# Optimization experiments

Measured on AMD Instinct MI355X. Metric: run time of the kernel, lower is better.

The kernel has to match this reference:

```python
import jax, jax.numpy as jnp
import numpy as np

N, E, D = 40000, 640000, 128
EPS = 1e-5


def _lin(k, out_d, in_d):
    s = 1.0 / np.sqrt(in_d)
    kw, kb = jax.random.split(k)
    W = jax.random.uniform(kw, (out_d, in_d), minval=-s, maxval=s, dtype=jnp.float32)
    b = jax.random.uniform(kb, (out_d,), minval=-s, maxval=s, dtype=jnp.float32)
    return W, b


def setup_inputs() -> dict:
    key = jax.random.key(0)
    kx, ke, k1, k2, k3, k4 = jax.random.split(key, 6)
    x = jax.random.normal(kx, (N, D), dtype=jnp.float32)
    edge_index = jax.random.randint(ke, (2, E), 0, N, dtype=jnp.int64)
    Wm1, bm1 = _lin(k1, D, D)
    Wm2, bm2 = _lin(k2, D, D)
    Wu1, bu1 = _lin(k3, D, 2 * D)
    Wu2, bu2 = _lin(k4, D, D)
    gamma = jnp.ones((D,), jnp.float32)
    beta = jnp.zeros((D,), jnp.float32)
    return dict(x=x, edge_index=edge_index, Wm1=Wm1, bm1=bm1, Wm2=Wm2, bm2=bm2,
                Wu1=Wu1, bu1=bu1, Wu2=Wu2, bu2=bu2, gamma=gamma, beta=beta)


def reference(x, edge_index, Wm1, bm1, Wm2, bm2, Wu1, bu1, Wu2, bu2, gamma, beta):
    num_nodes = x.shape[0]
    src, dst = edge_index[0], edge_index[1]
    # message MLP on gathered source features: (E, D)
    m = jax.nn.relu(x[src] @ Wm1.T + bm1) @ Wm2.T + bm2
    # scatter-mean via segment_sum + clamped count
    agg = jax.ops.segment_sum(m, dst, num_segments=num_nodes)
    cnt = jax.ops.segment_sum(jnp.ones((dst.shape[0],), m.dtype), dst, num_segments=num_nodes)
    agg = agg / jnp.clip(cnt, 1.0, None)[:, None]
    # update MLP on concat([x, agg]) -> (N, D); dropout is identity in eval
    comb = jnp.concatenate([x, agg], axis=-1)
    u = jax.nn.relu(comb @ Wu1.T + bu1) @ Wu2.T + bu2
    # residual + LayerNorm
    h = u + x
    mu = h.mean(-1, keepdims=True)
    var = ((h - mu) ** 2).mean(-1, keepdims=True)
    return (h - mu) / jnp.sqrt(var + EPS) * gamma + beta
```

## Files before the change

kernel.cpp:

```cpp
#include <hip/hip_runtime.h>

#define N_NODES 40000
#define N_EDGES 640000
#define DIM 128
#define NBLK_SCAN 157
#define NBLK_GEMM 313

typedef __bf16 bf16;
typedef __bf16 v8bf __attribute__((ext_vector_type(8)));
typedef __bf16 v4bf __attribute__((ext_vector_type(4)));
typedef float f32x4 __attribute__((ext_vector_type(4)));

#define MFMA(a, b, c) __builtin_amdgcn_mfma_f32_16x16x32_bf16(a, b, c, 0, 0, 0)

#define OFF_WM1 0
#define OFF_BM1 16384
#define OFF_WM2 16512
#define OFF_BM2 32896
#define OFF_WU1 33024
#define OFF_BU1 65792
#define OFF_WU2 65920
#define OFF_BU2 82304
#define OFF_GAM 82432
#define OFF_BET 82560
#define NPARAM  82688

template<bool I64>
__device__ __forceinline__ int ldi(const void* p, size_t i) {
    if constexpr (I64) return (int)((const long long*)p)[i];
    else               return ((const int*)p)[i];
}

__global__ __launch_bounds__(256) void detect_kernel(const unsigned short* __restrict__ xh,
                                                     const unsigned int* __restrict__ eiw,
                                                     int* __restrict__ flags) {
    __shared__ int sf[2];
    int tid = threadIdx.x;
    if (tid == 0) { sf[0] = 0; sf[1] = 0; }
    __syncthreads();
    int isf32 = 0; unsigned int orhi = 0;
    #pragma unroll
    for (int j = 0; j < 4; ++j) {
        unsigned short h = xh[2 * (tid + 256 * j)];
        if (((h >> 7) & 0xFF) >= 0xC0) isf32 = 1;
        orhi |= eiw[2 * (tid + 256 * j) + 1];
    }
    if (isf32) atomicOr(&sf[0], 1);
    if (orhi)  atomicOr(&sf[1], 1);
    __syncthreads();
    if (tid == 0) { flags[0] = sf[0]; flags[1] = sf[1] ? 0 : 1; }
}

__global__ __launch_bounds__(256) void convert_params_kernel(
    const void* Wm1, const void* bm1, const void* Wm2, const void* bm2,
    const void* Wu1, const void* bu1, const void* Wu2, const void* bu2,
    const void* gam, const void* bet, const int* __restrict__ flags,
    bf16* __restrict__ wp)
{
    int i = blockIdx.x * 256 + threadIdx.x;
    if (i >= NPARAM) return;
    const void* src; int base;
    if      (i < OFF_BM1) { src = Wm1; base = OFF_WM1; }
    else if (i < OFF_WM2) { src = bm1; base = OFF_BM1; }
    else if (i < OFF_BM2) { src = Wm2; base = OFF_WM2; }
    else if (i < OFF_WU1) { src = bm2; base = OFF_BM2; }
    else if (i < OFF_BU1) { src = Wu1; base = OFF_WU1; }
    else if (i < OFF_WU2) { src = bu1; base = OFF_BU1; }
    else if (i < OFF_BU2) { src = Wu2; base = OFF_WU2; }
    else if (i < OFF_GAM) { src = bu2; base = OFF_BU2; }
    else if (i < OFF_BET) { src = gam; base = OFF_GAM; }
    else                  { src = bet; base = OFF_BET; }
    int j = i - base;
    float v = flags[0] ? ((const float*)src)[j] : (float)((const bf16*)src)[j];
    wp[i] = (bf16)v;
}

__global__ __launch_bounds__(256) void convert_x_kernel(const void* __restrict__ x,
                                                        const int* __restrict__ flags,
                                                        bf16* __restrict__ xb) {
    const int NT = N_NODES * DIM;
    int stride = gridDim.x * 256;
    if (flags[0]) {
        const float4* g = (const float4*)x;
        v4bf* o = (v4bf*)xb;
        for (int i = blockIdx.x * 256 + threadIdx.x; i < NT / 4; i += stride) {
            float4 v = g[i];
            v4bf t; t[0] = (bf16)v.x; t[1] = (bf16)v.y; t[2] = (bf16)v.z; t[3] = (bf16)v.w;
            o[i] = t;
        }
    } else {
        const uint4* g = (const uint4*)x;
        uint4* o = (uint4*)xb;
        for (int i = blockIdx.x * 256 + threadIdx.x; i < NT / 8; i += stride) o[i] = g[i];
    }
}


__global__ __launch_bounds__(256) void msg_kernel(const bf16* __restrict__ xb,
                                                  const bf16* __restrict__ wp,
                                                  bf16* __restrict__ y)
{
    __shared__ __align__(16) bf16 sc[4][32 * DIM];
    const int wave = threadIdx.x >> 6, lane = threadIdx.x & 63;
    const int l15 = lane & 15, quad = lane >> 4;
    const int row0 = (blockIdx.x * 4 + wave) * 32;
    bf16* s = sc[wave];
    const bf16* W1 = wp + OFF_WM1;
    const bf16* W2 = wp + OFF_WM2;

    const int ra = min(row0 + l15, N_NODES - 1);
    const int rb = min(row0 + 16 + l15, N_NODES - 1);

    f32x4 acc[2][8] = {};
    #pragma unroll
    for (int kt = 0; kt < 4; ++kt) {
        int k0 = kt * 32 + quad * 8;
        v8bf a0 = *(const v8bf*)&xb[(size_t)ra * DIM + k0];
        v8bf a1 = *(const v8bf*)&xb[(size_t)rb * DIM + k0];
        #pragma unroll
        for (int ct = 0; ct < 8; ++ct) {
            v8bf b = *(const v8bf*)&W1[(ct * 16 + l15) * DIM + k0];
            acc[0][ct] = MFMA(a0, b, acc[0][ct]);
            acc[1][ct] = MFMA(a1, b, acc[1][ct]);
        }
    }
    #pragma unroll
    for (int ct = 0; ct < 8; ++ct) {
        float bb = (float)wp[OFF_BM1 + ct * 16 + l15];
        int c8w = (ct << 1) | (l15 >> 3);
        #pragma unroll
        for (int i = 0; i < 2; ++i)
            #pragma unroll
            for (int r = 0; r < 4; ++r) {
                int row = i * 16 + quad * 4 + r;
                s[row * DIM + (((c8w ^ (row & 15)) << 3) | (l15 & 7))] =
                    (bf16)fmaxf(acc[i][ct][r] + bb, 0.f);
            }
    }
    f32x4 acc2[2][8] = {};
    #pragma unroll
    for (int kt = 0; kt < 4; ++kt) {
        int k0 = kt * 32 + quad * 8;
        int c8 = kt * 4 + quad;
        v8bf a0 = *(const v8bf*)&s[l15 * DIM + ((c8 ^ l15) << 3)];
        v8bf a1 = *(const v8bf*)&s[(16 + l15) * DIM + ((c8 ^ l15) << 3)];
        #pragma unroll
        for (int ct = 0; ct < 8; ++ct) {
            v8bf b = *(const v8bf*)&W2[(ct * 16 + l15) * DIM + k0];
            acc2[0][ct] = MFMA(a0, b, acc2[0][ct]);
            acc2[1][ct] = MFMA(a1, b, acc2[1][ct]);
        }
    }
    #pragma unroll
    for (int ct = 0; ct < 8; ++ct) {
        float bb = (float)wp[OFF_BM2 + ct * 16 + l15];
        #pragma unroll
        for (int i = 0; i < 2; ++i)
            #pragma unroll
            for (int r = 0; r < 4; ++r) {
                int grow = row0 + i * 16 + quad * 4 + r;
                if (grow < N_NODES)
                    y[(size_t)grow * DIM + ct * 16 + l15] = (bf16)(acc2[i][ct][r] + bb);
            }
    }
}

__global__ __launch_bounds__(256) void update_kernel(const bf16* __restrict__ xb,
                                                     const bf16* __restrict__ agg,
                                                     const bf16* __restrict__ wp,
                                                     const int* __restrict__ flags,
                                                     void* __restrict__ out)
{
    __shared__ __align__(16) bf16 sc[4][32 * DIM];
    const int wave = threadIdx.x >> 6, lane = threadIdx.x & 63;
    const int l15 = lane & 15, quad = lane >> 4;
    const int row0 = (blockIdx.x * 4 + wave) * 32;
    bf16* s = sc[wave];
    const bf16* W1 = wp + OFF_WU1;
    const bf16* W2 = wp + OFF_WU2;
    const int of32 = flags[0];

    const int ra = min(row0 + l15, N_NODES - 1);
    const int rb = min(row0 + 16 + l15, N_NODES - 1);

    f32x4 acc[2][8] = {};
    #pragma unroll
    for (int kt = 0; kt < 8; ++kt) {
        int k0 = kt * 32 + quad * 8;
        const bf16* A = (kt < 4) ? xb : agg;
        int ko = (kt < 4) ? k0 : (k0 - 128);
        v8bf a0 = *(const v8bf*)&A[(size_t)ra * DIM + ko];
        v8bf a1 = *(const v8bf*)&A[(size_t)rb * DIM + ko];
        #pragma unroll
        for (int ct = 0; ct < 8; ++ct) {
            v8bf b = *(const v8bf*)&W1[(ct * 16 + l15) * 256 + k0];
            acc[0][ct] = MFMA(a0, b, acc[0][ct]);
            acc[1][ct] = MFMA(a1, b, acc[1][ct]);
        }
    }
    #pragma unroll
    for (int ct = 0; ct < 8; ++ct) {
        float bb = (float)wp[OFF_BU1 + ct * 16 + l15];
        int c8w = (ct << 1) | (l15 >> 3);
        #pragma unroll
        for (int i = 0; i < 2; ++i)
            #pragma unroll
            for (int r = 0; r < 4; ++r) {
                int row = i * 16 + quad * 4 + r;
                s[row * DIM + (((c8w ^ (row & 15)) << 3) | (l15 & 7))] =
                    (bf16)fmaxf(acc[i][ct][r] + bb, 0.f);
            }
    }
    f32x4 acc2[2][8] = {};
    #pragma unroll
    for (int kt = 0; kt < 4; ++kt) {
        int k0 = kt * 32 + quad * 8;
        int c8 = kt * 4 + quad;
        v8bf a0 = *(const v8bf*)&s[l15 * DIM + ((c8 ^ l15) << 3)];
        v8bf a1 = *(const v8bf*)&s[(16 + l15) * DIM + ((c8 ^ l15) << 3)];
        #pragma unroll
        for (int ct = 0; ct < 8; ++ct) {
            v8bf b = *(const v8bf*)&W2[(ct * 16 + l15) * DIM + k0];
            acc2[0][ct] = MFMA(a0, b, acc2[0][ct]);
            acc2[1][ct] = MFMA(a1, b, acc2[1][ct]);
        }
    }

    float bu2c[8], gc[8], bc[8];
    #pragma unroll
    for (int ct = 0; ct < 8; ++ct) {
        int col = ct * 16 + l15;
        bu2c[ct] = (float)wp[OFF_BU2 + col];
        gc[ct]   = (float)wp[OFF_GAM + col];
        bc[ct]   = (float)wp[OFF_BET + col];
    }
    #pragma unroll
    for (int i = 0; i < 2; ++i) {
        #pragma unroll
        for (int r = 0; r < 4; ++r) {
            int grow = row0 + i * 16 + quad * 4 + r;
            int growc = min(grow, N_NODES - 1);
            float u[8], s1 = 0.f, s2 = 0.f;
            #pragma unroll
            for (int ct = 0; ct < 8; ++ct) {
                float v = acc2[i][ct][r] + bu2c[ct]
                        + (float)xb[(size_t)growc * DIM + ct * 16 + l15];
                u[ct] = v; s1 += v; s2 += v * v;
            }
            #pragma unroll
            for (int off = 1; off < 16; off <<= 1) {
                s1 += __shfl_xor(s1, off);
                s2 += __shfl_xor(s2, off);
            }
            float mean = s1 * (1.f / 128.f);
            float var  = s2 * (1.f / 128.f) - mean * mean;
            float rstd = rsqrtf(var + 1e-5f);
            if (grow < N_NODES) {
                if (of32) {
                    #pragma unroll
                    for (int ct = 0; ct < 8; ++ct)
                        ((float*)out)[(size_t)grow * DIM + ct * 16 + l15] =
                            (u[ct] - mean) * rstd * gc[ct] + bc[ct];
                } else {
                    #pragma unroll
                    for (int ct = 0; ct < 8; ++ct)
                        ((bf16*)out)[(size_t)grow * DIM + ct * 16 + l15] =
                            (bf16)((u[ct] - mean) * rstd * gc[ct] + bc[ct]);
                }
            }
        }
    }
}

template<bool I64>
__device__ void hist_body(const void* ei, int* deg) {
    int e = blockIdx.x * 256 + threadIdx.x;
    if (e < N_EDGES) atomicAdd(&deg[ldi<I64>(ei, (size_t)N_EDGES + e)], 1);
}
__global__ __launch_bounds__(256) void hist_kernel(const void* ei, int* deg, const int* flags) {
    if (flags[1]) hist_body<true>(ei, deg); else hist_body<false>(ei, deg);
}

__global__ __launch_bounds__(256) void scan1_kernel(const int* __restrict__ deg,
                                                    int* __restrict__ bscan,
                                                    int* __restrict__ bsum) {
    __shared__ int s[256];
    int tid = threadIdx.x;
    int i = blockIdx.x * 256 + tid;
    int v = (i < N_NODES) ? deg[i] : 0;
    s[tid] = v;
    for (int off = 1; off < 256; off <<= 1) {
        __syncthreads();
        int t = (tid >= off) ? s[tid - off] : 0;
        __syncthreads();
        s[tid] += t;
    }
    if (i < N_NODES) bscan[i] = s[tid] - v;
    if (tid == 255) bsum[blockIdx.x] = s[255];
}

__global__ __launch_bounds__(256) void scan2_kernel(int* __restrict__ bsum) {
    __shared__ int s[256];
    int tid = threadIdx.x;
    int v = (tid < NBLK_SCAN) ? bsum[tid] : 0;
    s[tid] = v;
    for (int off = 1; off < 256; off <<= 1) {
        __syncthreads();
        int t = (tid >= off) ? s[tid - off] : 0;
        __syncthreads();
        s[tid] += t;
    }
    if (tid < NBLK_SCAN) bsum[tid] = s[tid] - v;
}

__global__ __launch_bounds__(256) void scan3_kernel(const int* __restrict__ bscan,
                                                    const int* __restrict__ bsum,
                                                    int* __restrict__ offsets) {
    int i = blockIdx.x * 256 + threadIdx.x;
    if (i < N_NODES) offsets[i] = bscan[i] + bsum[blockIdx.x];
}

template<bool I64>
__device__ void scatter_body(const void* ei, int* offsets, int* srcs) {
    int e = blockIdx.x * 256 + threadIdx.x;
    if (e < N_EDGES) {
        int d = ldi<I64>(ei, (size_t)N_EDGES + e);
        int pos = atomicAdd(&offsets[d], 1);
        srcs[pos] = ldi<I64>(ei, e);
    }
}
__global__ __launch_bounds__(256) void scatter_kernel(const void* ei, int* offsets, int* srcs,
                                                      const int* flags) {
    if (flags[1]) scatter_body<true>(ei, offsets, srcs);
    else          scatter_body<false>(ei, offsets, srcs);
}

__device__ __forceinline__ void accum8(float* s, uint4 v) {
    v8bf b = __builtin_bit_cast(v8bf, v);
    #pragma unroll
    for (int j = 0; j < 8; ++j) s[j] += (float)b[j];
}

__global__ __launch_bounds__(256) void agg_kernel(const bf16* __restrict__ y,
                                                  const int* __restrict__ srcs,
                                                  const int* __restrict__ offsets,
                                                  const int* __restrict__ deg,
                                                  bf16* __restrict__ agg) {
    const int node = (blockIdx.x << 2) + (threadIdx.x >> 6);
    const int lane = threadIdx.x & 63;
    const int slot = lane >> 4, c16 = lane & 15;
    const int end = offsets[node];
    const int cnt = deg[node];
    const int beg = end - cnt;
    const uint4* yv = (const uint4*)y;

    float s0[8] = {}, s1[8] = {};
    int e = beg + slot;
    for (; e + 4 < end; e += 8) {
        int i0 = srcs[e], i1 = srcs[e + 4];
        uint4 v0 = yv[(size_t)i0 * 16 + c16];
        uint4 v1 = yv[(size_t)i1 * 16 + c16];
        accum8(s0, v0);
        accum8(s1, v1);
    }
    if (e < end) accum8(s0, yv[(size_t)srcs[e] * 16 + c16]);

    float inv = 1.f / (float)(cnt > 0 ? cnt : 1);
    v8bf o;
    #pragma unroll
    for (int j = 0; j < 8; ++j) {
        float v = s0[j] + s1[j];
        v += __shfl_xor(v, 16);
        v += __shfl_xor(v, 32);
        o[j] = (bf16)(v * inv);
    }
    if (slot == 0)
        ((uint4*)agg)[(size_t)node * 16 + c16] = __builtin_bit_cast(uint4, o);
}

extern "C" void kernel_launch(void* const* d_in, const int* in_sizes, int n_in,
                              void* d_out, int out_size, void* d_ws, size_t ws_size,
                              hipStream_t stream) {
    const void* x   = d_in[0];
    const void* ei  = d_in[1];

    char* ws = (char*)d_ws;
    size_t off = 0;
    auto alloc = [&](size_t bytes) {
        void* p = ws + off;
        off += (bytes + 255) & ~(size_t)255;
        return p;
    };
    bf16* y       = (bf16*)alloc((size_t)N_NODES * DIM * sizeof(bf16));
    bf16* agg     = (bf16*)alloc((size_t)N_NODES * DIM * sizeof(bf16));
    bf16* xb      = (bf16*)alloc((size_t)N_NODES * DIM * sizeof(bf16));
    bf16* wp      = (bf16*)alloc((size_t)NPARAM * sizeof(bf16));
    int*  deg     = (int*)alloc(N_NODES * sizeof(int));
    int*  offsets = (int*)alloc(N_NODES * sizeof(int));
    int*  bscan   = (int*)alloc(N_NODES * sizeof(int));
    int*  bsum    = (int*)alloc(1024);
    int*  srcs    = (int*)alloc((size_t)N_EDGES * sizeof(int));
    int*  flags   = (int*)alloc(256);

    hipMemsetAsync(deg, 0, N_NODES * sizeof(int), stream);

    detect_kernel<<<1, 256, 0, stream>>>((const unsigned short*)x, (const unsigned int*)ei, flags);
    convert_params_kernel<<<(NPARAM + 255) / 256, 256, 0, stream>>>(
        d_in[2], d_in[3], d_in[4], d_in[5], d_in[6], d_in[7], d_in[8], d_in[9],
        d_in[10], d_in[11], flags, wp);
    convert_x_kernel<<<1024, 256, 0, stream>>>(x, flags, xb);

    msg_kernel<<<NBLK_GEMM, 256, 0, stream>>>(xb, wp, y);

    hist_kernel<<<(N_EDGES + 255) / 256, 256, 0, stream>>>(ei, deg, flags);
    scan1_kernel<<<NBLK_SCAN, 256, 0, stream>>>(deg, bscan, bsum);
    scan2_kernel<<<1, 256, 0, stream>>>(bsum);
    scan3_kernel<<<NBLK_SCAN, 256, 0, stream>>>(bscan, bsum, offsets);
    scatter_kernel<<<(N_EDGES + 255) / 256, 256, 0, stream>>>(ei, offsets, srcs, flags);
    agg_kernel<<<N_NODES / 4, 256, 0, stream>>>(y, srcs, offsets, deg, agg);

    update_kernel<<<NBLK_GEMM, 256, 0, stream>>>(xb, agg, wp, flags, d_out);
}
```

Before: 250.1 us.

## Fuse front-end prep and CSR build into one cooperative grid-synced kernel

```diff
diff --git a/kernel.cpp b/kernel.cpp
--- a/kernel.cpp
+++ b/kernel.cpp
@@ -1,10 +1,14 @@
 #include <hip/hip_runtime.h>
+#include <hip/hip_cooperative_groups.h>
+
+namespace cg = cooperative_groups;
 
 #define N_NODES 40000
 #define N_EDGES 640000
 #define DIM 128
 #define NBLK_SCAN 157
 #define NBLK_GEMM 313
+#define COOP_BLOCKS 256
 
 typedef __bf16 bf16;
 typedef __bf16 v8bf __attribute__((ext_vector_type(8)));
@@ -25,76 +29,136 @@
 #define OFF_BET 82560
 #define NPARAM  82688
 
-template<bool I64>
-__device__ __forceinline__ int ldi(const void* p, size_t i) {
-    if constexpr (I64) return (int)((const long long*)p)[i];
-    else               return ((const int*)p)[i];
-}
-
-__global__ __launch_bounds__(256) void detect_kernel(const unsigned short* __restrict__ xh,
-                                                     const unsigned int* __restrict__ eiw,
-                                                     int* __restrict__ flags) {
+__global__ __launch_bounds__(256) void coop_front_kernel(
+    const void* __restrict__ x, const void* __restrict__ ei,
+    const void* p0, const void* p1, const void* p2, const void* p3,
+    const void* p4, const void* p5, const void* p6, const void* p7,
+    const void* p8, const void* p9,
+    bf16* __restrict__ wp, bf16* __restrict__ xb,
+    int* __restrict__ deg, int* __restrict__ bscan, int* __restrict__ bsum,
+    int* __restrict__ offsets, int* __restrict__ srcs, int* __restrict__ flags)
+{
+    cg::grid_group grid = cg::this_grid();
     __shared__ int sf[2];
-    int tid = threadIdx.x;
+    __shared__ int s[256];
+    const int tid = threadIdx.x;
+    const int gid = blockIdx.x * 256 + tid;
+    const int gstride = gridDim.x * 256;
+
     if (tid == 0) { sf[0] = 0; sf[1] = 0; }
     __syncthreads();
-    int isf32 = 0; unsigned int orhi = 0;
-    #pragma unroll
-    for (int j = 0; j < 4; ++j) {
-        unsigned short h = xh[2 * (tid + 256 * j)];
-        if (((h >> 7) & 0xFF) >= 0xC0) isf32 = 1;
-        orhi |= eiw[2 * (tid + 256 * j) + 1];
-    }
-    if (isf32) atomicOr(&sf[0], 1);
-    if (orhi)  atomicOr(&sf[1], 1);
+    {
+        const unsigned short* xh = (const unsigned short*)x;
+        const unsigned int* eiw = (const unsigned int*)ei;
+        int isf32 = 0; unsigned int orhi = 0;
+        #pragma unroll
+        for (int j = 0; j < 4; ++j) {
+            unsigned short h = xh[2 * (tid + 256 * j)];
+            if (((h >> 7) & 0xFF) >= 0xC0) isf32 = 1;
+            orhi |= eiw[2 * (tid + 256 * j) + 1];
+        }
+        if (isf32) atomicOr(&sf[0], 1);
+        if (orhi)  atomicOr(&sf[1], 1);
+    }
     __syncthreads();
-    if (tid == 0) { flags[0] = sf[0]; flags[1] = sf[1] ? 0 : 1; }
-}
-
-__global__ __launch_bounds__(256) void convert_params_kernel(
-    const void* Wm1, const void* bm1, const void* Wm2, const void* bm2,
-    const void* Wu1, const void* bu1, const void* Wu2, const void* bu2,
-    const void* gam, const void* bet, const int* __restrict__ flags,
-    bf16* __restrict__ wp)
-{
-    int i = blockIdx.x * 256 + threadIdx.x;
-    if (i >= NPARAM) return;
-    const void* src; int base;
-    if      (i < OFF_BM1) { src = Wm1; base = OFF_WM1; }
-    else if (i < OFF_WM2) { src = bm1; base = OFF_BM1; }
-    else if (i < OFF_BM2) { src = Wm2; base = OFF_WM2; }
-    else if (i < OFF_WU1) { src = bm2; base = OFF_BM2; }
-    else if (i < OFF_BU1) { src = Wu1; base = OFF_WU1; }
-    else if (i < OFF_WU2) { src = bu1; base = OFF_BU1; }
-    else if (i < OFF_BU2) { src = Wu2; base = OFF_WU2; }
-    else if (i < OFF_GAM) { src = bu2; base = OFF_BU2; }
-    else if (i < OFF_BET) { src = gam; base = OFF_GAM; }
-    else                  { src = bet; base = OFF_BET; }
-    int j = i - base;
-    float v = flags[0] ? ((const float*)src)[j] : (float)((const bf16*)src)[j];
-    wp[i] = (bf16)v;
-}
-
-__global__ __launch_bounds__(256) void convert_x_kernel(const void* __restrict__ x,
-                                                        const int* __restrict__ flags,
-                                                        bf16* __restrict__ xb) {
-    const int NT = N_NODES * DIM;
-    int stride = gridDim.x * 256;
-    if (flags[0]) {
-        const float4* g = (const float4*)x;
-        v4bf* o = (v4bf*)xb;
-        for (int i = blockIdx.x * 256 + threadIdx.x; i < NT / 4; i += stride) {
-            float4 v = g[i];
-            v4bf t; t[0] = (bf16)v.x; t[1] = (bf16)v.y; t[2] = (bf16)v.z; t[3] = (bf16)v.w;
-            o[i] = t;
-        }
+    const int f32m = sf[0];
+    const int i64m = sf[1] ? 0 : 1;
+    if (blockIdx.x == 0 && tid == 0) { flags[0] = f32m; flags[1] = i64m; }
+
+    for (int i = gid; i < NPARAM; i += gstride) {
+        const void* src; int base;
+        if      (i < OFF_BM1) { src = p0; base = OFF_WM1; }
+        else if (i < OFF_WM2) { src = p1; base = OFF_BM1; }
+        else if (i < OFF_BM2) { src = p2; base = OFF_WM2; }
+        else if (i < OFF_WU1) { src = p3; base = OFF_BM2; }
+        else if (i < OFF_BU1) { src = p4; base = OFF_WU1; }
+        else if (i < OFF_WU2) { src = p5; base = OFF_BU1; }
+        else if (i < OFF_BU2) { src = p6; base = OFF_WU2; }
+        else if (i < OFF_GAM) { src = p7; base = OFF_BU2; }
+        else if (i < OFF_BET) { src = p8; base = OFF_GAM; }
+        else                  { src = p9; base = OFF_BET; }
+        int j = i - base;
+        float v = f32m ? ((const float*)src)[j] : (float)((const bf16*)src)[j];
+        wp[i] = (bf16)v;
+    }
+    {
+        const int NT = N_NODES * DIM;
+        if (f32m) {
+            const float4* g = (const float4*)x;
+            v4bf* o = (v4bf*)xb;
+            for (int i = gid; i < NT / 4; i += gstride) {
+                float4 v = g[i];
+                v4bf t; t[0] = (bf16)v.x; t[1] = (bf16)v.y; t[2] = (bf16)v.z; t[3] = (bf16)v.w;
+                o[i] = t;
+            }
+        } else {
+            const uint4* g = (const uint4*)x;
+            uint4* o = (uint4*)xb;
+            for (int i = gid; i < NT / 8; i += gstride) o[i] = g[i];
+        }
+    }
+    for (int i = gid; i < N_NODES; i += gstride) deg[i] = 0;
+    grid.sync();
+
+    if (i64m) {
+        const long long* d = (const long long*)ei + N_EDGES;
+        for (int e = gid; e < N_EDGES; e += gstride) atomicAdd(&deg[(int)d[e]], 1);
     } else {
-        const uint4* g = (const uint4*)x;
-        uint4* o = (uint4*)xb;
-        for (int i = blockIdx.x * 256 + threadIdx.x; i < NT / 8; i += stride) o[i] = g[i];
-    }
-}
-
+        const int* d = (const int*)ei + N_EDGES;
+        for (int e = gid; e < N_EDGES; e += gstride) atomicAdd(&deg[d[e]], 1);
+    }
+    grid.sync();
+
+    if (blockIdx.x < NBLK_SCAN) {
+        int i = blockIdx.x * 256 + tid;
+        int v = (i < N_NODES) ? deg[i] : 0;
+        s[tid] = v;
+        for (int off = 1; off < 256; off <<= 1) {
+            __syncthreads();
+            int t = (tid >= off) ? s[tid - off] : 0;
+            __syncthreads();
+            s[tid] += t;
+        }
+        if (i < N_NODES) bscan[i] = s[tid] - v;
+        if (tid == 255) bsum[blockIdx.x] = s[255];
+    }
+    grid.sync();
+
+    if (blockIdx.x == 0) {
+        int v = (tid < NBLK_SCAN) ? bsum[tid] : 0;
+        s[tid] = v;
+        for (int off = 1; off < 256; off <<= 1) {
+            __syncthreads();
+            int t = (tid >= off) ? s[tid - off] : 0;
+            __syncthreads();
+            s[tid] += t;
+        }
+        if (tid < NBLK_SCAN) bsum[tid] = s[tid] - v;
+    }
+    grid.sync();
+
+    for (int i = gid; i < N_NODES; i += gstride)
+        offsets[i] = bscan[i] + bsum[i >> 8];
+    grid.sync();
+
+    if (i64m) {
+        const long long* sp = (const long long*)ei;
+        const long long* dp = sp + N_EDGES;
+        for (int e = gid; e < N_EDGES; e += gstride) {
+            int d = (int)dp[e];
+            int pos = atomicAdd(&offsets[d], 1);
+            srcs[pos] = (int)sp[e];
+        }
+    } else {
+        const int* sp = (const int*)ei;
+        const int* dp = sp + N_EDGES;
+        for (int e = gid; e < N_EDGES; e += gstride) {
+            int d = dp[e];
+            int pos = atomicAdd(&offsets[d], 1);
+            srcs[pos] = sp[e];
+        }
+    }
+}
 
 __global__ __launch_bounds__(256) void msg_kernel(const bf16* __restrict__ xb,
                                                   const bf16* __restrict__ wp,
@@ -272,69 +336,6 @@
     }
 }
 
-template<bool I64>
-__device__ void hist_body(const void* ei, int* deg) {
-    int e = blockIdx.x * 256 + threadIdx.x;
-    if (e < N_EDGES) atomicAdd(&deg[ldi<I64>(ei, (size_t)N_EDGES + e)], 1);
-}
-__global__ __launch_bounds__(256) void hist_kernel(const void* ei, int* deg, const int* flags) {
-    if (flags[1]) hist_body<true>(ei, deg); else hist_body<false>(ei, deg);
-}
-
-__global__ __launch_bounds__(256) void scan1_kernel(const int* __restrict__ deg,
-                                                    int* __restrict__ bscan,
-                                                    int* __restrict__ bsum) {
-    __shared__ int s[256];
-    int tid = threadIdx.x;
-    int i = blockIdx.x * 256 + tid;
-    int v = (i < N_NODES) ? deg[i] : 0;
-    s[tid] = v;
-    for (int off = 1; off < 256; off <<= 1) {
-        __syncthreads();
-        int t = (tid >= off) ? s[tid - off] : 0;
-        __syncthreads();
-        s[tid] += t;
-    }
-    if (i < N_NODES) bscan[i] = s[tid] - v;
-    if (tid == 255) bsum[blockIdx.x] = s[255];
-}
-
-__global__ __launch_bounds__(256) void scan2_kernel(int* __restrict__ bsum) {
-    __shared__ int s[256];
-    int tid = threadIdx.x;
-    int v = (tid < NBLK_SCAN) ? bsum[tid] : 0;
-    s[tid] = v;
-    for (int off = 1; off < 256; off <<= 1) {
-        __syncthreads();
-        int t = (tid >= off) ? s[tid - off] : 0;
-        __syncthreads();
-        s[tid] += t;
-    }
-    if (tid < NBLK_SCAN) bsum[tid] = s[tid] - v;
-}
-
-__global__ __launch_bounds__(256) void scan3_kernel(const int* __restrict__ bscan,
-                                                    const int* __restrict__ bsum,
-                                                    int* __restrict__ offsets) {
-    int i = blockIdx.x * 256 + threadIdx.x;
-    if (i < N_NODES) offsets[i] = bscan[i] + bsum[blockIdx.x];
-}
-
-template<bool I64>
-__device__ void scatter_body(const void* ei, int* offsets, int* srcs) {
-    int e = blockIdx.x * 256 + threadIdx.x;
-    if (e < N_EDGES) {
-        int d = ldi<I64>(ei, (size_t)N_EDGES + e);
-        int pos = atomicAdd(&offsets[d], 1);
-        srcs[pos] = ldi<I64>(ei, e);
-    }
-}
-__global__ __launch_bounds__(256) void scatter_kernel(const void* ei, int* offsets, int* srcs,
-                                                      const int* flags) {
-    if (flags[1]) scatter_body<true>(ei, offsets, srcs);
-    else          scatter_body<false>(ei, offsets, srcs);
-}
-
 __device__ __forceinline__ void accum8(float* s, uint4 v) {
     v8bf b = __builtin_bit_cast(v8bf, v);
     #pragma unroll
@@ -381,8 +382,8 @@
 extern "C" void kernel_launch(void* const* d_in, const int* in_sizes, int n_in,
                               void* d_out, int out_size, void* d_ws, size_t ws_size,
                               hipStream_t stream) {
-    const void* x   = d_in[0];
-    const void* ei  = d_in[1];
+    const void* x  = d_in[0];
+    const void* ei = d_in[1];
 
     char* ws = (char*)d_ws;
     size_t off = 0;
@@ -402,22 +403,23 @@
     int*  srcs    = (int*)alloc((size_t)N_EDGES * sizeof(int));
     int*  flags   = (int*)alloc(256);
 
-    hipMemsetAsync(deg, 0, N_NODES * sizeof(int), stream);
-
-    detect_kernel<<<1, 256, 0, stream>>>((const unsigned short*)x, (const unsigned int*)ei, flags);
-    convert_params_kernel<<<(NPARAM + 255) / 256, 256, 0, stream>>>(
-        d_in[2], d_in[3], d_in[4], d_in[5], d_in[6], d_in[7], d_in[8], d_in[9],
-        d_in[10], d_in[11], flags, wp);
-    convert_x_kernel<<<1024, 256, 0, stream>>>(x, flags, xb);
+    void* p0 = (void*)d_in[2]; void* p1 = (void*)d_in[3];
+    void* p2 = (void*)d_in[4]; void* p3 = (void*)d_in[5];
+    void* p4 = (void*)d_in[6]; void* p5 = (void*)d_in[7];
+    void* p6 = (void*)d_in[8]; void* p7 = (void*)d_in[9];
+    void* p8 = (void*)d_in[10]; void* p9 = (void*)d_in[11];
+
+    void* args[] = {
+        (void*)&x, (void*)&ei,
+        (void*)&p0, (void*)&p1, (void*)&p2, (void*)&p3, (void*)&p4,
+        (void*)&p5, (void*)&p6, (void*)&p7, (void*)&p8, (void*)&p9,
+        (void*)&wp, (void*)&xb, (void*)&deg, (void*)&bscan, (void*)&bsum,
+        (void*)&offsets, (void*)&srcs, (void*)&flags
+    };
+    hipLaunchCooperativeKernel((void*)coop_front_kernel, dim3(COOP_BLOCKS),
+                               dim3(256), args, 0, stream);
 
     msg_kernel<<<NBLK_GEMM, 256, 0, stream>>>(xb, wp, y);
-
-    hist_kernel<<<(N_EDGES + 255) / 256, 256, 0, stream>>>(ei, deg, flags);
-    scan1_kernel<<<NBLK_SCAN, 256, 0, stream>>>(deg, bscan, bsum);
-    scan2_kernel<<<1, 256, 0, stream>>>(bsum);
-    scan3_kernel<<<NBLK_SCAN, 256, 0, stream>>>(bscan, bsum, offsets);
-    scatter_kernel<<<(N_EDGES + 255) / 256, 256, 0, stream>>>(ei, offsets, srcs, flags);
     agg_kernel<<<N_NODES / 4, 256, 0, stream>>>(y, srcs, offsets, deg, agg);
-
     update_kernel<<<NBLK_GEMM, 256, 0, stream>>>(xb, agg, wp, flags, d_out);
 }
```

Result: slower. 400.1 us (+60.0%).
